# Kernel tuning notes

Hardware: AMD Instinct MI355X
Metric: run time of the kernel (lower is better)

## Reference

```python
import jax, jax.numpy as jnp
import numpy as np

N_NODES = 50000
N_EDGES = 1600000
IN_DIM = 128
HEADS = 8
OUT_C = 16  # per-head channels; HEADS*OUT_C == IN_DIM -> residual active
NEG_SLOPE = 0.2
BN_EPS = 1e-5


def setup_inputs() -> dict:
    key = jax.random.key(0)
    ks = jax.random.split(key, 8)
    x = jax.random.normal(ks[0], (N_NODES, IN_DIM), dtype=jnp.float32)
    edge_index = jax.random.randint(ks[1], (2, N_EDGES), 0, N_NODES, dtype=jnp.int64)
    # GATConv params (PyG: shared lin for src/dst on single-tensor input)
    W = jax.random.normal(ks[2], (IN_DIM, HEADS * OUT_C), dtype=jnp.float32) / np.sqrt(IN_DIM)
    att_src = jax.random.normal(ks[3], (HEADS, OUT_C), dtype=jnp.float32) / np.sqrt(OUT_C)
    att_dst = jax.random.normal(ks[4], (HEADS, OUT_C), dtype=jnp.float32) / np.sqrt(OUT_C)
    bias = jnp.zeros((HEADS * OUT_C,), dtype=jnp.float32)
    # BatchNorm1d affine params
    gamma = jnp.ones((HEADS * OUT_C,), dtype=jnp.float32)
    beta = jnp.zeros((HEADS * OUT_C,), dtype=jnp.float32)
    return {"x": x, "edge_index": edge_index, "W": W, "att_src": att_src,
            "att_dst": att_dst, "bias": bias, "gamma": gamma, "beta": beta}


def reference(x, edge_index, W, att_src, att_dst, bias, gamma, beta):
    N = x.shape[0]
    H, C = att_src.shape
    src, dst = edge_index[0], edge_index[1]

    xl = (x @ W).reshape(N, H, C)                      # [N,H,C]
    a_src = jnp.sum(xl * att_src[None], axis=-1)       # [N,H]
    a_dst = jnp.sum(xl * att_dst[None], axis=-1)       # [N,H]

    e = jax.nn.leaky_relu(a_src[src] + a_dst[dst], NEG_SLOPE)  # [E,H]
    # segment softmax over incoming edges of each dst node
    m = jax.ops.segment_max(e, dst, num_segments=N)    # [N,H], -inf for empty
    m = jnp.where(jnp.isfinite(m), m, 0.0)
    ex = jnp.exp(e - m[dst])                           # [E,H]
    denom = jax.ops.segment_sum(ex, dst, num_segments=N)
    alpha = ex / (denom[dst] + 1e-16)                  # [E,H]

    out = jax.ops.segment_sum(alpha[:, :, None] * xl[src], dst, num_segments=N)  # [N,H,C]
    h = out.reshape(N, H * C) + bias

    # BatchNorm1d (training mode: batch statistics, biased variance)
    mean = jnp.mean(h, axis=0)
    var = jnp.mean((h - mean) ** 2, axis=0)
    h = (h - mean) * jax.lax.rsqrt(var + BN_EPS) * gamma + beta

    h = jax.nn.relu(h)
    return x + h  # residual (in_dim == H*C)
```

## Files before the change

kernel.cpp:

```cpp
#include <hip/hip_runtime.h>
#include <hip/hip_fp16.h>
#include <math.h>

#define N_NODES 50000
#define N_EDGES 1600000
#define DIM 128
#define HEADS 8
#define NEG_SLOPE 0.2f
#define BN_EPS 1e-5f

typedef _Float16 f16x8 __attribute__((ext_vector_type(8)));
typedef float f32x4 __attribute__((ext_vector_type(4)));

__global__ void k_wprep(const float* __restrict__ W, __half* __restrict__ Wh,
                        int* __restrict__ bcur, float* __restrict__ gsums) {
    const int t = threadIdx.x;
    if (blockIdx.x == 0 && t < 256) bcur[t] = 0;
    if (blockIdx.x == 1 && t < 256) gsums[t] = 0.f;
    const int tid = blockIdx.x * 256 + t;
    const int g = tid >> 6;
    const int lane = tid & 63;
    const int nt = g >> 2, kt = g & 3;
    const int q = lane >> 4, n = lane & 15;
    #pragma unroll
    for (int j = 0; j < 8; ++j)
        Wh[(size_t)(g * 64 + lane) * 8 + j] =
            __float2half(W[(kt * 32 + q * 8 + j) * DIM + nt * 16 + n]);
}

__global__ __launch_bounds__(256) void k_lin(const float* __restrict__ x,
                      const __half* __restrict__ Wh, const float* __restrict__ att_s,
                      const float* __restrict__ att_d, __half* __restrict__ xlh,
                      float* __restrict__ a_src, float* __restrict__ a_dst) {
    const int wave = threadIdx.x >> 6;
    const int lane = threadIdx.x & 63;
    const int q = lane >> 4, n = lane & 15;
    const int nb = (blockIdx.x * 4 + wave) * 16;

    const int rowA = min(nb + n, N_NODES - 1);
    const float* xr = x + (size_t)rowA * DIM;
    f16x8 a[4];
    #pragma unroll
    for (int kt = 0; kt < 4; ++kt) {
        const float4 p0 = *(const float4*)(xr + kt * 32 + q * 8);
        const float4 p1 = *(const float4*)(xr + kt * 32 + q * 8 + 4);
        a[kt][0] = (_Float16)p0.x; a[kt][1] = (_Float16)p0.y;
        a[kt][2] = (_Float16)p0.z; a[kt][3] = (_Float16)p0.w;
        a[kt][4] = (_Float16)p1.x; a[kt][5] = (_Float16)p1.y;
        a[kt][6] = (_Float16)p1.z; a[kt][7] = (_Float16)p1.w;
    }

    f32x4 acc[8];
    #pragma unroll
    for (int nt = 0; nt < 8; ++nt) acc[nt] = (f32x4){0.f, 0.f, 0.f, 0.f};

    const f16x8* wb = (const f16x8*)Wh;
    #pragma unroll
    for (int nt = 0; nt < 8; ++nt) {
        #pragma unroll
        for (int kt = 0; kt < 4; ++kt) {
            const f16x8 b = wb[(nt * 4 + kt) * 64 + lane];
            acc[nt] = __builtin_amdgcn_mfma_f32_16x16x32_f16(a[kt], b, acc[nt], 0, 0, 0);
        }
    }

    const int r0 = nb + q * 4;
    #pragma unroll
    for (int nt = 0; nt < 8; ++nt) {
        const float as = att_s[nt * 16 + n];
        const float ad = att_d[nt * 16 + n];
        #pragma unroll
        for (int r = 0; r < 4; ++r) {
            const int row = r0 + r;
            const float v = acc[nt][r];
            float s = v * as;
            float d = v * ad;
            #pragma unroll
            for (int off = 8; off; off >>= 1) {
                s += __shfl_xor(s, off, 16);
                d += __shfl_xor(d, off, 16);
            }
            if (row < N_NODES) {
                xlh[(size_t)row * DIM + nt * 16 + n] = __float2half(v);
                if (n == 0) {
                    a_src[row * HEADS + nt] = s;
                    a_dst[row * HEADS + nt] = d;
                }
            }
        }
    }
}

#define SCAN_B 256
#define NBUCK 196
#define SEGCAP 12288
#define CHUNK 8192
#define NB_A ((N_EDGES + CHUNK - 1) / CHUNK)

__global__ __launch_bounds__(256) void k_binA(const int* __restrict__ ei,
                                              int* __restrict__ bcur,
                                              unsigned int* __restrict__ pairs) {
    __shared__ int hist[NBUCK], excl[NBUCK], gbase[NBUCK], cnt2[NBUCK];
    __shared__ int sc[SCAN_B];
    __shared__ unsigned int buf[CHUNK];
    const int t = threadIdx.x;
    const int base = blockIdx.x * CHUNK;
    const int cnt = min(CHUNK, N_EDGES - base);

    for (int j = t; j < NBUCK; j += 256) { hist[j] = 0; cnt2[j] = 0; }
    __syncthreads();
    for (int i = t * 4; i < cnt; i += 1024) {
        const int4 dv = *(const int4*)(ei + N_EDGES + base + i);
        atomicAdd(&hist[dv.x >> 8], 1);
        atomicAdd(&hist[dv.y >> 8], 1);
        atomicAdd(&hist[dv.z >> 8], 1);
        atomicAdd(&hist[dv.w >> 8], 1);
    }
    __syncthreads();
    sc[t] = (t < NBUCK) ? hist[t] : 0;
    __syncthreads();
    for (int d = 1; d < SCAN_B; d <<= 1) {
        const int xo = (t >= d) ? sc[t - d] : 0;
        __syncthreads();
        sc[t] += xo;
        __syncthreads();
    }
    if (t < NBUCK) {
        excl[t] = sc[t] - hist[t];
        gbase[t] = t * SEGCAP + atomicAdd(&bcur[t], hist[t]);
    }
    __syncthreads();
    for (int i = t * 4; i < cnt; i += 1024) {
        const int4 sv = *(const int4*)(ei + base + i);
        const int4 dv = *(const int4*)(ei + N_EDGES + base + i);
        const int ss[4] = {sv.x, sv.y, sv.z, sv.w};
        const int dd[4] = {dv.x, dv.y, dv.z, dv.w};
        #pragma unroll
        for (int k = 0; k < 4; ++k) {
            const int b = dd[k] >> 8;
            const int r = atomicAdd(&cnt2[b], 1);
            buf[excl[b] + r] = (unsigned int)ss[k] | ((unsigned int)(dd[k] & 255) << 16)
                             | ((unsigned int)b << 24);
        }
    }
    __syncthreads();
    for (int i = t; i < cnt; i += 256) {
        const unsigned int u = buf[i];
        const int b = u >> 24;
        pairs[gbase[b] + (i - excl[b])] = u & 0xFFFFFF;
    }
}

__global__ __launch_bounds__(512) void k_binB(const unsigned int* __restrict__ pairs,
                                              const int* __restrict__ bcur,
                                              unsigned short* __restrict__ csr,
                                              int2* __restrict__ nrange) {
    __shared__ int hist[256], excl[256], cnt2[256];
    __shared__ unsigned short out[SEGCAP];
    const int t = threadIdx.x;
    const int b = blockIdx.x;
    const int lo = b * SEGCAP;
    const int cnt = bcur[b];

    if (t < 256) { hist[t] = 0; cnt2[t] = 0; }
    __syncthreads();
    for (int i = t; i < cnt; i += 512)
        atomicAdd(&hist[pairs[lo + i] >> 16], 1);
    __syncthreads();
    if (t < 256) excl[t] = hist[t];
    __syncthreads();
    for (int d = 1; d < 256; d <<= 1) {
        int xo = 0;
        if (t < 256 && t >= d) xo = excl[t - d];
        __syncthreads();
        if (t < 256) excl[t] += xo;
        __syncthreads();
    }
    if (t < 256) excl[t] -= hist[t];
    __syncthreads();
    for (int i = t; i < cnt; i += 512) {
        const unsigned int u = pairs[lo + i];
        const int dl = u >> 16;
        const int r = atomicAdd(&cnt2[dl], 1);
        out[excl[dl] + r] = (unsigned short)(u & 0xFFFF);
    }
    __syncthreads();
    for (int i = t; i < cnt; i += 512)
        csr[2 * lo + i] = out[i];
    if (t < 256) {
        const int node = (b << 8) + t;
        if (node < N_NODES) {
            int2 rg;
            rg.x = 2 * lo + excl[t];
            rg.y = rg.x + hist[t];
            nrange[node] = rg;
        }
    }
}

#define AGG_NPW 8
#define AGG_NB  ((N_NODES + 4 * AGG_NPW - 1) / (4 * AGG_NPW))

__global__ __launch_bounds__(256) void k_aggr4(const int2* __restrict__ nrange,
                        const unsigned short* __restrict__ csr,
                        const float* __restrict__ a_src, const float* __restrict__ a_dst,
                        const __half* __restrict__ xlh, const float* __restrict__ bias,
                        float* __restrict__ y, float* __restrict__ partials) {
    __shared__ float ch_s[DIM], ch_ss[DIM];
    const int t = threadIdx.x;
    const int wave = t >> 6, lane = t & 63;
    const int c2 = lane << 1;
    const int h = lane >> 3;
    if (t < DIM) { ch_s[t] = 0.f; ch_ss[t] = 0.f; }
    __syncthreads();

    const float b0 = bias[c2], b1 = bias[c2 + 1];
    float ps0 = 0.f, pss0 = 0.f, ps1 = 0.f, pss1 = 0.f;

    const int nb = (blockIdx.x * 4 + wave) * AGG_NPW;
    for (int ii = 0; ii < AGG_NPW; ++ii) {
        const int d = nb + ii;
        if (d >= N_NODES) break;
        const int2 rg = nrange[d];
        const int lo = rg.x, hi = rg.y;
        const float ad = a_dst[d * HEADS + h];
        float acc0 = 0.f, acc1 = 0.f, dsum = 0.f;
        int i = lo;
        for (; i + 8 <= hi; i += 8) {
            int s[8];
            float e[8];
            __half2 xv[8];
            #pragma unroll
            for (int j = 0; j < 8; ++j) s[j] = csr[i + j];
            #pragma unroll
            for (int j = 0; j < 8; ++j) e[j] = a_src[s[j] * HEADS + h] + ad;
            #pragma unroll
            for (int j = 0; j < 8; ++j)
                xv[j] = *(const __half2*)(xlh + (size_t)s[j] * DIM + c2);
            #pragma unroll
            for (int j = 0; j < 8; ++j) {
                const float w = __expf(fmaxf(e[j], NEG_SLOPE * e[j]));
                const float2 f = __half22float2(xv[j]);
                acc0 = fmaf(w, f.x, acc0);
                acc1 = fmaf(w, f.y, acc1);
                dsum += w;
            }
        }
        for (; i < hi; ++i) {
            const int s = csr[i];
            const float e = a_src[s * HEADS + h] + ad;
            const __half2 xv = *(const __half2*)(xlh + (size_t)s * DIM + c2);
            const float w = __expf(fmaxf(e, NEG_SLOPE * e));
            const float2 f = __half22float2(xv);
            acc0 = fmaf(w, f.x, acc0); acc1 = fmaf(w, f.y, acc1); dsum += w;
        }
        const float inv = 1.f / (dsum + 1e-16f);
        const float o0 = acc0 * inv, o1 = acc1 * inv;
        float2 o; o.x = o0; o.y = o1;
        *(float2*)(y + (size_t)d * DIM + c2) = o;
        const float h0 = o0 + b0, h1 = o1 + b1;
        ps0 += h0; pss0 += h0 * h0;
        ps1 += h1; pss1 += h1 * h1;
    }
    atomicAdd(&ch_s[c2], ps0);      atomicAdd(&ch_s[c2 + 1], ps1);
    atomicAdd(&ch_ss[c2], pss0);    atomicAdd(&ch_ss[c2 + 1], pss1);
    __syncthreads();
    partials[(size_t)blockIdx.x * 256 + t] = (t < DIM) ? ch_s[t] : ch_ss[t - DIM];
}

#define NRED 16
__global__ void k_red(const float* __restrict__ partials, float* __restrict__ gsums) {
    const int t = threadIdx.x;
    float v = 0.f;
    for (int r = blockIdx.x; r < AGG_NB; r += NRED)
        v += partials[(size_t)r * 256 + t];
    atomicAdd(&gsums[t], v);
}

__global__ void k_statfin(const float* __restrict__ sums, const float* __restrict__ sumsq,
                          const float* __restrict__ gamma, const float* __restrict__ beta,
                          const float* __restrict__ bias, float* __restrict__ scale,
                          float* __restrict__ shift) {
    const int c = threadIdx.x;
    const float inv_n = 1.f / (float)N_NODES;
    const float mean = sums[c] * inv_n;
    const float var = sumsq[c] * inv_n - mean * mean;
    const float sc = rsqrtf(var + BN_EPS) * gamma[c];
    scale[c] = sc;
    shift[c] = beta[c] + (bias[c] - mean) * sc;
}

__global__ void k_final(float* __restrict__ y, const float* __restrict__ x,
                        const float* __restrict__ scale, const float* __restrict__ shift) {
    const int q = blockIdx.x * blockDim.x + threadIdx.x;
    const int cq = q & (DIM / 4 - 1);
    float4 v = ((const float4*)y)[q];
    const float4 xv = ((const float4*)x)[q];
    const float4 sc = ((const float4*)scale)[cq];
    const float4 sh = ((const float4*)shift)[cq];
    v.x = xv.x + fmaxf(v.x * sc.x + sh.x, 0.f);
    v.y = xv.y + fmaxf(v.y * sc.y + sh.y, 0.f);
    v.z = xv.z + fmaxf(v.z * sc.z + sh.z, 0.f);
    v.w = xv.w + fmaxf(v.w * sc.w + sh.w, 0.f);
    ((float4*)y)[q] = v;
}

extern "C" void kernel_launch(void* const* d_in, const int* in_sizes, int n_in,
                              void* d_out, int out_size, void* d_ws, size_t ws_size,
                              hipStream_t stream) {
    const float* x     = (const float*)d_in[0];
    const int*   ei    = (const int*)  d_in[1];
    const float* W     = (const float*)d_in[2];
    const float* att_s = (const float*)d_in[3];
    const float* att_d = (const float*)d_in[4];
    const float* bias  = (const float*)d_in[5];
    const float* gamma = (const float*)d_in[6];
    const float* beta  = (const float*)d_in[7];
    float* y = (float*)d_out;

    __half* xlh  = (__half*)d_ws;
    float* a_src = (float*)(xlh + (size_t)N_NODES * DIM);
    float* a_dst = a_src + (size_t)N_NODES * HEADS;
    float* sums  = a_dst + (size_t)N_NODES * HEADS;
    float* sumsq = sums  + DIM;
    float* scale = sumsq + DIM;
    float* shift = scale + DIM;
    int*   bcur  = (int*)(shift + DIM);
    int2*  nrange = (int2*)(bcur + 256);
    __half* Wh   = (__half*)(nrange + N_NODES);
    unsigned int* pairs = (unsigned int*)(Wh + 16384);
    unsigned short* csr = (unsigned short*)pairs;
    float* partials = (float*)(pairs + (size_t)NBUCK * SEGCAP);

    k_wprep<<<8, 256, 0, stream>>>(W, Wh, bcur, sums);
    k_lin<<<(N_NODES + 63) / 64, 256, 0, stream>>>(x, Wh, att_s, att_d, xlh, a_src, a_dst);
    k_binA<<<NB_A, 256, 0, stream>>>(ei, bcur, pairs);
    k_binB<<<NBUCK, 512, 0, stream>>>(pairs, bcur, csr, nrange);
    k_aggr4<<<AGG_NB, 256, 0, stream>>>(nrange, csr, a_src, a_dst, xlh, bias, y, partials);
    k_red<<<NRED, 256, 0, stream>>>(partials, sums);
    k_statfin<<<1, DIM, 0, stream>>>(sums, sumsq, gamma, beta, bias, scale, shift);
    k_final<<<(size_t)N_NODES * DIM / 4 / 256, 256, 0, stream>>>(y, x, scale, shift);
}
```

Measured before the change: 249.5 us.

## Fuse BN stats into aggregation atomics, vectorize CSR loads, widen binning blocks

```diff
diff --git a/kernel.cpp b/kernel.cpp
--- a/kernel.cpp
+++ b/kernel.cpp
@@ -91,25 +91,24 @@
     }
 }
 
-#define SCAN_B 256
 #define NBUCK 196
 #define SEGCAP 12288
 #define CHUNK 8192
 #define NB_A ((N_EDGES + CHUNK - 1) / CHUNK)
 
-__global__ __launch_bounds__(256) void k_binA(const int* __restrict__ ei,
-                                              int* __restrict__ bcur,
-                                              unsigned int* __restrict__ pairs) {
+__global__ __launch_bounds__(1024) void k_binA(const int* __restrict__ ei,
+                                               int* __restrict__ bcur,
+                                               unsigned int* __restrict__ pairs) {
     __shared__ int hist[NBUCK], excl[NBUCK], gbase[NBUCK], cnt2[NBUCK];
-    __shared__ int sc[SCAN_B];
+    __shared__ int sc[256];
     __shared__ unsigned int buf[CHUNK];
     const int t = threadIdx.x;
     const int base = blockIdx.x * CHUNK;
     const int cnt = min(CHUNK, N_EDGES - base);
 
-    for (int j = t; j < NBUCK; j += 256) { hist[j] = 0; cnt2[j] = 0; }
-    __syncthreads();
-    for (int i = t * 4; i < cnt; i += 1024) {
+    for (int j = t; j < NBUCK; j += 1024) { hist[j] = 0; cnt2[j] = 0; }
+    __syncthreads();
+    for (int i = t * 4; i < cnt; i += 4096) {
         const int4 dv = *(const int4*)(ei + N_EDGES + base + i);
         atomicAdd(&hist[dv.x >> 8], 1);
         atomicAdd(&hist[dv.y >> 8], 1);
@@ -117,12 +116,13 @@
         atomicAdd(&hist[dv.w >> 8], 1);
     }
     __syncthreads();
-    sc[t] = (t < NBUCK) ? hist[t] : 0;
-    __syncthreads();
-    for (int d = 1; d < SCAN_B; d <<= 1) {
-        const int xo = (t >= d) ? sc[t - d] : 0;
+    if (t < 256) sc[t] = (t < NBUCK) ? hist[t] : 0;
+    __syncthreads();
+    for (int d = 1; d < 256; d <<= 1) {
+        int xo = 0;
+        if (t < 256 && t >= d) xo = sc[t - d];
         __syncthreads();
-        sc[t] += xo;
+        if (t < 256) sc[t] += xo;
         __syncthreads();
     }
     if (t < NBUCK) {
@@ -130,7 +130,7 @@
         gbase[t] = t * SEGCAP + atomicAdd(&bcur[t], hist[t]);
     }
     __syncthreads();
-    for (int i = t * 4; i < cnt; i += 1024) {
+    for (int i = t * 4; i < cnt; i += 4096) {
         const int4 sv = *(const int4*)(ei + base + i);
         const int4 dv = *(const int4*)(ei + N_EDGES + base + i);
         const int ss[4] = {sv.x, sv.y, sv.z, sv.w};
@@ -144,18 +144,19 @@
         }
     }
     __syncthreads();
-    for (int i = t; i < cnt; i += 256) {
+    for (int i = t; i < cnt; i += 1024) {
         const unsigned int u = buf[i];
         const int b = u >> 24;
         pairs[gbase[b] + (i - excl[b])] = u & 0xFFFFFF;
     }
 }
 
-__global__ __launch_bounds__(512) void k_binB(const unsigned int* __restrict__ pairs,
-                                              const int* __restrict__ bcur,
-                                              unsigned short* __restrict__ csr,
-                                              int2* __restrict__ nrange) {
-    __shared__ int hist[256], excl[256], cnt2[256];
+__global__ __launch_bounds__(1024) void k_binB(const unsigned int* __restrict__ pairs,
+                                               const int* __restrict__ bcur,
+                                               unsigned short* __restrict__ csr,
+                                               int2* __restrict__ nrange) {
+    __shared__ int hist[256], eh[256], excl[256], cnt2[256];
+    __shared__ int plen;
     __shared__ unsigned short out[SEGCAP];
     const int t = threadIdx.x;
     const int b = blockIdx.x;
@@ -164,10 +165,10 @@
 
     if (t < 256) { hist[t] = 0; cnt2[t] = 0; }
     __syncthreads();
-    for (int i = t; i < cnt; i += 512)
+    for (int i = t; i < cnt; i += 1024)
         atomicAdd(&hist[pairs[lo + i] >> 16], 1);
     __syncthreads();
-    if (t < 256) excl[t] = hist[t];
+    if (t < 256) { eh[t] = (hist[t] + 1) & ~1; excl[t] = eh[t]; }
     __syncthreads();
     for (int d = 1; d < 256; d <<= 1) {
         int xo = 0;
@@ -176,16 +177,18 @@
         if (t < 256) excl[t] += xo;
         __syncthreads();
     }
-    if (t < 256) excl[t] -= hist[t];
-    __syncthreads();
-    for (int i = t; i < cnt; i += 512) {
+    if (t < 256) excl[t] -= eh[t];
+    if (t == 255) plen = excl[255] + eh[255];
+    __syncthreads();
+    for (int i = t; i < cnt; i += 1024) {
         const unsigned int u = pairs[lo + i];
         const int dl = u >> 16;
         const int r = atomicAdd(&cnt2[dl], 1);
         out[excl[dl] + r] = (unsigned short)(u & 0xFFFF);
     }
     __syncthreads();
-    for (int i = t; i < cnt; i += 512)
+    const int pl = plen;
+    for (int i = t; i < pl; i += 1024)
         csr[2 * lo + i] = out[i];
     if (t < 256) {
         const int node = (b << 8) + t;
@@ -198,14 +201,14 @@
     }
 }
 
-#define AGG_NPW 8
-#define AGG_NB  ((N_NODES + 4 * AGG_NPW - 1) / (4 * AGG_NPW))
+#define AGG_NPW 4
+#define AGG_NB  (N_NODES / (4 * AGG_NPW))
 
 __global__ __launch_bounds__(256) void k_aggr4(const int2* __restrict__ nrange,
                         const unsigned short* __restrict__ csr,
                         const float* __restrict__ a_src, const float* __restrict__ a_dst,
                         const __half* __restrict__ xlh, const float* __restrict__ bias,
-                        float* __restrict__ y, float* __restrict__ partials) {
+                        float* __restrict__ y, float* __restrict__ gsums) {
     __shared__ float ch_s[DIM], ch_ss[DIM];
     const int t = threadIdx.x;
     const int wave = t >> 6, lane = t & 63;
@@ -218,20 +221,23 @@
     float ps0 = 0.f, pss0 = 0.f, ps1 = 0.f, pss1 = 0.f;
 
     const int nb = (blockIdx.x * 4 + wave) * AGG_NPW;
+    #pragma unroll
     for (int ii = 0; ii < AGG_NPW; ++ii) {
         const int d = nb + ii;
-        if (d >= N_NODES) break;
         const int2 rg = nrange[d];
         const int lo = rg.x, hi = rg.y;
         const float ad = a_dst[d * HEADS + h];
         float acc0 = 0.f, acc1 = 0.f, dsum = 0.f;
         int i = lo;
         for (; i + 8 <= hi; i += 8) {
+            const int4 sp = *(const int4*)(csr + i);
             int s[8];
+            s[0] = sp.x & 0xFFFF; s[1] = ((unsigned)sp.x) >> 16;
+            s[2] = sp.y & 0xFFFF; s[3] = ((unsigned)sp.y) >> 16;
+            s[4] = sp.z & 0xFFFF; s[5] = ((unsigned)sp.z) >> 16;
+            s[6] = sp.w & 0xFFFF; s[7] = ((unsigned)sp.w) >> 16;
             float e[8];
             __half2 xv[8];
-            #pragma unroll
-            for (int j = 0; j < 8; ++j) s[j] = csr[i + j];
             #pragma unroll
             for (int j = 0; j < 8; ++j) e[j] = a_src[s[j] * HEADS + h] + ad;
             #pragma unroll
@@ -265,43 +271,30 @@
     atomicAdd(&ch_s[c2], ps0);      atomicAdd(&ch_s[c2 + 1], ps1);
     atomicAdd(&ch_ss[c2], pss0);    atomicAdd(&ch_ss[c2 + 1], pss1);
     __syncthreads();
-    partials[(size_t)blockIdx.x * 256 + t] = (t < DIM) ? ch_s[t] : ch_ss[t - DIM];
-}
-
-#define NRED 16
-__global__ void k_red(const float* __restrict__ partials, float* __restrict__ gsums) {
-    const int t = threadIdx.x;
-    float v = 0.f;
-    for (int r = blockIdx.x; r < AGG_NB; r += NRED)
-        v += partials[(size_t)r * 256 + t];
-    atomicAdd(&gsums[t], v);
-}
-
-__global__ void k_statfin(const float* __restrict__ sums, const float* __restrict__ sumsq,
-                          const float* __restrict__ gamma, const float* __restrict__ beta,
-                          const float* __restrict__ bias, float* __restrict__ scale,
-                          float* __restrict__ shift) {
-    const int c = threadIdx.x;
-    const float inv_n = 1.f / (float)N_NODES;
-    const float mean = sums[c] * inv_n;
-    const float var = sumsq[c] * inv_n - mean * mean;
-    const float sc = rsqrtf(var + BN_EPS) * gamma[c];
-    scale[c] = sc;
-    shift[c] = beta[c] + (bias[c] - mean) * sc;
+    atomicAdd(&gsums[t], (t < DIM) ? ch_s[t] : ch_ss[t - DIM]);
 }
 
 __global__ void k_final(float* __restrict__ y, const float* __restrict__ x,
-                        const float* __restrict__ scale, const float* __restrict__ shift) {
+                        const float* __restrict__ sums, const float* __restrict__ sumsq,
+                        const float* __restrict__ gamma, const float* __restrict__ beta,
+                        const float* __restrict__ bias) {
     const int q = blockIdx.x * blockDim.x + threadIdx.x;
     const int cq = q & (DIM / 4 - 1);
+    const float4 sm = ((const float4*)sums)[cq];
+    const float4 sq = ((const float4*)sumsq)[cq];
+    const float4 gm = ((const float4*)gamma)[cq];
+    const float4 bt = ((const float4*)beta)[cq];
+    const float4 bs = ((const float4*)bias)[cq];
     float4 v = ((const float4*)y)[q];
     const float4 xv = ((const float4*)x)[q];
-    const float4 sc = ((const float4*)scale)[cq];
-    const float4 sh = ((const float4*)shift)[cq];
-    v.x = xv.x + fmaxf(v.x * sc.x + sh.x, 0.f);
-    v.y = xv.y + fmaxf(v.y * sc.y + sh.y, 0.f);
-    v.z = xv.z + fmaxf(v.z * sc.z + sh.z, 0.f);
-    v.w = xv.w + fmaxf(v.w * sc.w + sh.w, 0.f);
+    const float inv_n = 1.f / (float)N_NODES;
+#define BNC(c) { const float mean = sm.c * inv_n;                         \
+                 const float var = sq.c * inv_n - mean * mean;            \
+                 const float sc = rsqrtf(var + BN_EPS) * gm.c;            \
+                 const float sh = bt.c + (bs.c - mean) * sc;              \
+                 v.c = xv.c + fmaxf(v.c * sc + sh, 0.f); }
+    BNC(x) BNC(y) BNC(z) BNC(w)
+#undef BNC
     ((float4*)y)[q] = v;
 }
 
@@ -323,21 +316,17 @@
     float* a_dst = a_src + (size_t)N_NODES * HEADS;
     float* sums  = a_dst + (size_t)N_NODES * HEADS;
     float* sumsq = sums  + DIM;
-    float* scale = sumsq + DIM;
-    float* shift = scale + DIM;
-    int*   bcur  = (int*)(shift + DIM);
+    int*   bcur  = (int*)(sumsq + DIM);
     int2*  nrange = (int2*)(bcur + 256);
     __half* Wh   = (__half*)(nrange + N_NODES);
     unsigned int* pairs = (unsigned int*)(Wh + 16384);
     unsigned short* csr = (unsigned short*)pairs;
-    float* partials = (float*)(pairs + (size_t)NBUCK * SEGCAP);
 
     k_wprep<<<8, 256, 0, stream>>>(W, Wh, bcur, sums);
     k_lin<<<(N_NODES + 63) / 64, 256, 0, stream>>>(x, Wh, att_s, att_d, xlh, a_src, a_dst);
-    k_binA<<<NB_A, 256, 0, stream>>>(ei, bcur, pairs);
-    k_binB<<<NBUCK, 512, 0, stream>>>(pairs, bcur, csr, nrange);
-    k_aggr4<<<AGG_NB, 256, 0, stream>>>(nrange, csr, a_src, a_dst, xlh, bias, y, partials);
-    k_red<<<NRED, 256, 0, stream>>>(partials, sums);
-    k_statfin<<<1, DIM, 0, stream>>>(sums, sumsq, gamma, beta, bias, scale, shift);
-    k_final<<<(size_t)N_NODES * DIM / 4 / 256, 256, 0, stream>>>(y, x, scale, shift);
-}
+    k_binA<<<NB_A, 1024, 0, stream>>>(ei, bcur, pairs);
+    k_binB<<<NBUCK, 1024, 0, stream>>>(pairs, bcur, csr, nrange);
+    k_aggr4<<<AGG_NB, 256, 0, stream>>>(nrange, csr, a_src, a_dst, xlh, bias, y, sums);
+    k_final<<<(size_t)N_NODES * DIM / 4 / 256, 256, 0, stream>>>(y, x, sums, sumsq,
+                                                                 gamma, beta, bias);
+}
```

Result: slower. 258.4 us (+3.5%).
